# Optimization experiments

Measured on AMD Instinct MI355X. Metric: run time of the kernel, lower is better.

## Reference

```python
import jax, jax.numpy as jnp
import numpy as np

N = 4096
E = 262144
IN_DIM = 256
EDGE_DIM = 16
NUM_ATOM_FEATURES = 16
LATENT_DIM = 128
NUM_BOND_TYPES = 5


def setup_inputs() -> dict:
    key = jax.random.key(0)
    ks = jax.random.split(key, 12)
    inp = {
        's': jax.random.normal(ks[0], (N, IN_DIM), dtype=jnp.float32),
        'e': jax.random.normal(ks[1], (E, EDGE_DIM), dtype=jnp.float32),
        'batch': jnp.zeros((N,), dtype=jnp.int64),
        'edge_index_global': jax.random.randint(ks[2], (2, E), 0, N, dtype=jnp.int64),
        # learned parameters (torch nn.Linear layout: W is [out, in])
        'W_shared': jax.random.normal(ks[3], (IN_DIM, IN_DIM), dtype=jnp.float32) * 0.02,
        'b_shared': jnp.zeros((IN_DIM,), dtype=jnp.float32),
        'W_bond': jax.random.normal(ks[4], (IN_DIM, EDGE_DIM), dtype=jnp.float32) * 0.02,
        'b_bond': jnp.zeros((IN_DIM,), dtype=jnp.float32),
        'W_bonds': jax.random.normal(ks[5], (NUM_BOND_TYPES, IN_DIM), dtype=jnp.float32) * 0.02,
        'b_bonds': jnp.zeros((NUM_BOND_TYPES,), dtype=jnp.float32),
        'W_atoms': jax.random.normal(ks[6], (NUM_ATOM_FEATURES + LATENT_DIM, IN_DIM), dtype=jnp.float32) * 0.02,
        'b_atoms': jnp.zeros((NUM_ATOM_FEATURES + LATENT_DIM,), dtype=jnp.float32),
    }
    return inp


def reference(s, e, batch, edge_index_global,
              W_shared, b_shared, W_bond, b_bond,
              W_bonds, b_bonds, W_atoms, b_atoms):
    # shared_mapping: Linear + SiLU
    s = jax.nn.silu(s @ W_shared.T + b_shared)  # [n, in_dim]
    j = edge_index_global[0]
    i = edge_index_global[1]
    n = s.shape[0]

    # atoms_lin then split into atom-type logits and latent prediction
    atoms_out = s @ W_atoms.T + b_atoms  # [n, num_atom_features + latent_dim]
    atoms_pred = atoms_out[:, :NUM_ATOM_FEATURES]
    latent_pred = atoms_out[:, NUM_ATOM_FEATURES:]

    # dense scatter -> symmetrize -> gather (faithful to the original O(n^2) path)
    e_dense = jnp.zeros((n, n, e.shape[-1]), dtype=e.dtype).at[j, i].set(e)
    e_dense = 0.5 * (e_dense + e_dense.transpose(1, 0, 2))
    e_sym = e_dense[j, i]  # [E, edge_dim]

    # fused gather + bond linear + SiLU + bonds linear
    f = jax.nn.silu(s[i] + s[j] + e_sym @ W_bond.T + b_bond)  # [E, in_dim]
    bonds_pred = f @ W_bonds.T + b_bonds  # [E, num_bond_types]

    return (latent_pred, atoms_pred, bonds_pred)
```

## Files before the change

### kernel.cpp

```cpp
#include <hip/hip_runtime.h>
#include <hip/hip_bf16.h>

#define N_NODES   4096
#define E_EDGES   262144
#define IN_DIM    256
#define EDGE_DIM  16
#define NAF       16
#define LATENT    128
#define NBT       5

#define LATENT_OFF 0
#define ATOMS_OFF  (N_NODES * LATENT)
#define BONDS_OFF  (ATOMS_OFF + N_NODES * NAF)

#define TBITS 20
#define TSIZE (1u << TBITS)
#define TMASK (TSIZE - 1u)

typedef float    f32x4  __attribute__((ext_vector_type(4)));
typedef float    f32x4v __attribute__((ext_vector_type(4)));
typedef short    bf16x8 __attribute__((ext_vector_type(8)));
typedef unsigned u32x2  __attribute__((ext_vector_type(2)));
typedef unsigned u32x4  __attribute__((ext_vector_type(4)));

__device__ __forceinline__ float silu_f(float x) {
    return x * __builtin_amdgcn_rcpf(1.0f + __expf(-x));
}

__device__ __forceinline__ unsigned pack_bf16x2(float lo, float hi) {
#if __has_builtin(__builtin_amdgcn_cvt_pk_bf16_f32)
    typedef __bf16 bf16x2_t __attribute__((ext_vector_type(2)));
    union { bf16x2_t v; unsigned u; } c;
    c.v = __builtin_amdgcn_cvt_pk_bf16_f32(lo, hi);
    return c.u;
#else
    union { float f; unsigned u; } a, b;
    a.f = lo; b.f = hi;
    const unsigned ra = (a.u + 0x7FFFu + ((a.u >> 16) & 1u)) >> 16;
    const unsigned rb = (b.u + 0x7FFFu + ((b.u >> 16) & 1u)) >> 16;
    return ra | (rb << 16);
#endif
}

__device__ __forceinline__ float bf_lo(unsigned u) {
    union { unsigned x; float f; } c; c.x = u << 16; return c.f;
}
__device__ __forceinline__ float bf_hi(unsigned u) {
    union { unsigned x; float f; } c; c.x = u & 0xFFFF0000u; return c.f;
}

__device__ __forceinline__ void split_bf16(const float4 x0, const float4 x1,
                                           bf16x8* hi, bf16x8* lo) {
    union { bf16x8 v; unsigned u[4]; } H, L;
    H.u[0] = pack_bf16x2(x0.x, x0.y);
    H.u[1] = pack_bf16x2(x0.z, x0.w);
    H.u[2] = pack_bf16x2(x1.x, x1.y);
    H.u[3] = pack_bf16x2(x1.z, x1.w);
    L.u[0] = pack_bf16x2(x0.x - bf_lo(H.u[0]), x0.y - bf_hi(H.u[0]));
    L.u[1] = pack_bf16x2(x0.z - bf_lo(H.u[1]), x0.w - bf_hi(H.u[1]));
    L.u[2] = pack_bf16x2(x1.x - bf_lo(H.u[2]), x1.y - bf_hi(H.u[2]));
    L.u[3] = pack_bf16x2(x1.z - bf_lo(H.u[3]), x1.w - bf_hi(H.u[3]));
    *hi = H.v; *lo = L.v;
}

__device__ __forceinline__ void gld_lds16(const void* g, void* l) {
    __builtin_amdgcn_global_load_lds(
        (const __attribute__((address_space(1))) unsigned*)g,
        (__attribute__((address_space(3))) unsigned*)l, 16, 0, 0);
}

__device__ __forceinline__ unsigned hashh(unsigned key) {
    return (key * 2654435761u) >> (32 - TBITS);
}

__device__ __forceinline__ int resolve2(const unsigned long long* __restrict__ tab,
                                        unsigned key, unsigned long long s0,
                                        unsigned long long s1, unsigned h) {
    if ((unsigned)(s0 >> 18) == key + 1u) return (int)(s0 & 0x3FFFFu);
    if (s0 == 0ULL) return -1;
    if ((unsigned)(s1 >> 18) == key + 1u) return (int)(s1 & 0x3FFFFu);
    if (s1 == 0ULL) return -1;
    h = (h + 2u) & TMASK;
    while (true) {
        const unsigned long long cur = tab[h];
        if (cur == 0ULL) return -1;
        if ((unsigned)(cur >> 18) == key + 1u) return (int)(cur & 0x3FFFFu);
        h = (h + 1u) & TMASK;
    }
}

__global__ __launch_bounds__(256) void k_front(const float* __restrict__ s,
                                               const float* __restrict__ Wsh,
                                               const float* __restrict__ bsh,
                                               const int* __restrict__ eidx,
                                               const float* __restrict__ Wb,
                                               const float* __restrict__ bb,
                                               const float* __restrict__ Wbs,
                                               unsigned short* __restrict__ sact16,
                                               unsigned long long* __restrict__ tab,
                                               u32x4* __restrict__ A1pre,
                                               u32x4* __restrict__ A2pre) {
    const int blk = blockIdx.x;
    const int c   = threadIdx.x;

    if (blk >= 1024) {
        if (blk < 2048) {
            const int k = (blk - 1024) * 256 + c;
            const unsigned j = (unsigned)eidx[k];
            const unsigned i = (unsigned)eidx[E_EDGES + k];
            const unsigned key = (j << 12) | i;
            const unsigned long long mine =
                ((unsigned long long)(key + 1u) << 18) | (unsigned)k;
            unsigned h = hashh(key);
            while (true) {
                unsigned long long cur = tab[h];
                if (cur == 0ULL) {
                    const unsigned long long old = atomicCAS(&tab[h], 0ULL, mine);
                    if (old == 0ULL) return;
                    cur = old;
                }
                if ((unsigned)(cur >> 18) == key + 1u) {
                    atomicMax(&tab[h], mine);
                    return;
                }
                h = (h + 1u) & TMASK;
            }
        } else {
#pragma unroll
            for (int ee = 0; ee < 4; ++ee) {
                const int idx  = c + 256 * ee;
                const int g    = idx >> 6;
                const int lane = idx & 63;
                const int mm   = lane & 15;
                const int qq   = lane >> 4;

                const float4 w = *(const float4*)(Wb + (16 * g + mm) * EDGE_DIM + 4 * qq);
                u32x4 r1;
                r1.x = pack_bf16x2(w.x, w.y);
                r1.y = pack_bf16x2(w.z, w.w);
                r1.z = pack_bf16x2(bb[16 * g + mm], 0.0f);
                r1.w = 0u;
                A1pre[idx] = r1;

                u32x4 r2;
                if (mm < NBT) {
                    const float4 ws = *(const float4*)(Wbs + mm * IN_DIM + 16 * g + 4 * qq);
                    r2.x = pack_bf16x2(ws.x, ws.y);
                    r2.y = pack_bf16x2(ws.z, ws.w);
                } else {
                    r2.x = 0u; r2.y = 0u;
                }
                r2.z = 0u; r2.w = 0u;
                A2pre[idx] = r2;
            }
        }
        return;
    }

    const int lane = c & 63;
    const int wv   = c >> 6;
    const int wave = blk * 4 + wv;
    const int m    = lane & 15;
    const int q    = lane >> 4;
    const int row0 = (wave >> 4) * 16;
    const int col0 = (wave & 15) * 16;

    f32x4v acc;
    {
        const float bias = bsh[col0 + m];
        acc[0] = bias; acc[1] = bias; acc[2] = bias; acc[3] = bias;
    }

    const float* ap = s   + (size_t)(row0 + m) * IN_DIM + 8 * q;
    const float* bp = Wsh + (size_t)(col0 + m) * IN_DIM + 8 * q;

#pragma unroll
    for (int c8 = 0; c8 < 8; ++c8) {
        const float4 a0 = *(const float4*)(ap + 32 * c8);
        const float4 a1 = *(const float4*)(ap + 32 * c8 + 4);
        const float4 b0 = *(const float4*)(bp + 32 * c8);
        const float4 b1 = *(const float4*)(bp + 32 * c8 + 4);
        bf16x8 Ah, Al, Bh, Bl;
        split_bf16(a0, a1, &Ah, &Al);
        split_bf16(b0, b1, &Bh, &Bl);
        acc = __builtin_amdgcn_mfma_f32_16x16x32_bf16(Ah, Bh, acc, 0, 0, 0);
        acc = __builtin_amdgcn_mfma_f32_16x16x32_bf16(Al, Bh, acc, 0, 0, 0);
        acc = __builtin_amdgcn_mfma_f32_16x16x32_bf16(Ah, Bl, acc, 0, 0, 0);
    }

#pragma unroll
    for (int r = 0; r < 4; ++r) {
        const int row = row0 + 4 * q + r;
        const float v = silu_f(acc[r]);
        sact16[(size_t)row * IN_DIM + col0 + m] =
            (unsigned short)(pack_bf16x2(v, 0.0f) & 0xFFFFu);
    }
}

#define SB0()    __builtin_amdgcn_sched_barrier(0)
#define LGKM0()  do { __asm__ __volatile__("s_waitcnt lgkmcnt(0)" ::: "memory"); SB0(); } while (0)
#define VMW(n)   do { __asm__ __volatile__("s_waitcnt vmcnt(" #n ")" ::: "memory"); SB0(); } while (0)

__global__ __launch_bounds__(256, 5) void k_edges_mfma(const int* __restrict__ eidx,
                                                       const float* __restrict__ e,
                                                       const unsigned long long* __restrict__ tab,
                                                       const unsigned short* __restrict__ sact16,
                                                       const u32x4* __restrict__ A1pre,
                                                       const u32x4* __restrict__ A2pre,
                                                       const float* __restrict__ bbs,
                                                       const float* __restrict__ Wa,
                                                       const float* __restrict__ ba,
                                                       float* __restrict__ out) {
    __shared__ unsigned lds_all[4][2048];
    const int blk  = blockIdx.x;
    const int lane = threadIdx.x & 63;
    const int wv   = threadIdx.x >> 6;
    const int m    = lane & 15;
    const int q    = lane >> 4;

    if (blk >= 4096) {
        const int wave = (blk - 4096) * 4 + wv;
        const int rt = wave / 9;
        const int ct = wave - rt * 9;
        const int row0  = rt * 16;
        const int n_abs = ct * 16 + m;

        f32x4v acc;
        {
            const float bias = ba[n_abs];
            acc[0] = bias; acc[1] = bias; acc[2] = bias; acc[3] = bias;
        }

        const unsigned short* apu = sact16 + (size_t)(row0 + m) * IN_DIM + 8 * q;
        const float*          bp  = Wa + (size_t)n_abs * IN_DIM + 8 * q;

#pragma unroll
        for (int c8 = 0; c8 < 8; ++c8) {
            const bf16x8 A = *(const bf16x8*)(apu + 32 * c8);
            const float4 b0 = *(const float4*)(bp + 32 * c8);
            const float4 b1 = *(const float4*)(bp + 32 * c8 + 4);
            bf16x8 Bh, Bl;
            split_bf16(b0, b1, &Bh, &Bl);
            acc = __builtin_amdgcn_mfma_f32_16x16x32_bf16(A, Bh, acc, 0, 0, 0);
            acc = __builtin_amdgcn_mfma_f32_16x16x32_bf16(A, Bl, acc, 0, 0, 0);
        }
#pragma unroll
        for (int r = 0; r < 4; ++r) {
            const int row = row0 + 4 * q + r;
            if (n_abs < NAF)
                out[ATOMS_OFF + (size_t)row * NAF + n_abs] = acc[r];
            else
                out[LATENT_OFF + (size_t)row * LATENT + (n_abs - NAF)] = acc[r];
        }
        return;
    }

    const int k0 = __builtin_amdgcn_readfirstlane((blk * 4 + wv) * 16);
    unsigned* myl = lds_all[wv];
    const short one_q0 = (q == 0) ? (short)0x3F80 : (short)0;

    f32x4v acc_init;
#pragma unroll
    for (int r = 0; r < 4; ++r) {
        const int bond = 4 * q + r;
        acc_init[r] = (bond < NBT) ? bbs[bond] : 0.0f;
    }
    const u32x4* a1p = A1pre + lane;
    const u32x4* a2p = A2pre + lane;
    const int qh = q >> 1;
    const int qw = 2 * (q & 1);
    const int mw = m * 4;

    const unsigned j_m = (unsigned)eidx[k0 + m];
    const unsigned i_m = (unsigned)eidx[E_EDGES + k0 + m];

    const char* si_base = (const char*)(sact16 + (size_t)i_m * IN_DIM);
    const char* sj_base = (const char*)(sact16 + (size_t)j_m * IN_DIM);

    const unsigned keyF = (j_m << 12) | i_m, keyR = (i_m << 12) | j_m;
    const unsigned hF = hashh(keyF), hR = hashh(keyR);
    const unsigned long long sF0 = tab[hF];
    const unsigned long long sF1 = tab[(hF + 1u) & TMASK];
    const unsigned long long sR0 = tab[hR];
    const unsigned long long sR1 = tab[(hR + 1u) & TMASK];

    auto stage_q = [&](int p, int qb) {
        gld_lds16(si_base + p * 128 + (q)     * 16, (char*)myl + qb);
        gld_lds16(si_base + p * 128 + (4 + q) * 16, (char*)myl + qb + 1024);
        gld_lds16(sj_base + p * 128 + (q)     * 16, (char*)myl + qb + 2048);
        gld_lds16(sj_base + p * 128 + (4 + q) * 16, (char*)myl + qb + 3072);
        SB0();
    };

    stage_q(0, 0);
    stage_q(1, 4096);

    const int wf = resolve2(tab, keyF, sF0, sF1, hF);
    const int wr = resolve2(tab, keyR, sR0, sR1, hR);

    const float rsc = (wr >= 0) ? 0.5f : 0.0f;
    const int   wrc = (wr >= 0) ? wr : 0;
    const f32x4 ef = *(const f32x4*)(e + (size_t)wf  * EDGE_DIM + 4 * q);
    const f32x4 er = *(const f32x4*)(e + (size_t)wrc * EDGE_DIM + 4 * q);

    union { bf16x8 v; short s[8]; unsigned u[4]; } B1;
    {
        const f32x4 es = ef * 0.5f + er * rsc;
        B1.u[0] = pack_bf16x2(es[0], es[1]);
        B1.u[1] = pack_bf16x2(es[2], es[3]);
        B1.s[4] = one_q0; B1.s[5] = 0;
        B1.u[3] = 0u;
    }

    f32x4v acc0 = acc_init;
    f32x4v acc1 = {0.0f, 0.0f, 0.0f, 0.0f};

    auto qcompute = [&](int qb4, int gbase) {
#pragma unroll
        for (int gp = 0; gp < 4; ++gp) {
            const int g   = gbase + gp;
            const int cl  = 2 * gp + qh;
            const int off = (cl >> 2) * 256 + (cl & 3) * 64 + mw + qw;

            const u32x2 wi = *(const u32x2*)(myl + qb4 + off);
            const u32x2 wj = *(const u32x2*)(myl + qb4 + 512 + off);

            f32x4v C1;
            C1[0] = bf_lo(wi.x) + bf_lo(wj.x);
            C1[1] = bf_hi(wi.x) + bf_hi(wj.x);
            C1[2] = bf_lo(wi.y) + bf_lo(wj.y);
            C1[3] = bf_hi(wi.y) + bf_hi(wj.y);

            const u32x4 r1 = a1p[g * 64];
            const u32x4 r2 = a2p[g * 64];
            union { bf16x8 v; unsigned u[4]; } A1, A2;
            A1.u[0] = r1.x; A1.u[1] = r1.y; A1.u[2] = r1.z; A1.u[3] = 0u;
            A2.u[0] = r2.x; A2.u[1] = r2.y; A2.u[2] = 0u;   A2.u[3] = 0u;

            const f32x4v P = __builtin_amdgcn_mfma_f32_16x16x32_bf16(A1.v, B1.v, C1, 0, 0, 0);

            union { bf16x8 v; unsigned u[4]; } B2;
            B2.u[0] = pack_bf16x2(silu_f(P[0]), silu_f(P[1]));
            B2.u[1] = pack_bf16x2(silu_f(P[2]), silu_f(P[3]));
            B2.u[2] = 0u; B2.u[3] = 0u;

            if (gp & 1) acc1 = __builtin_amdgcn_mfma_f32_16x16x32_bf16(A2.v, B2.v, acc1, 0, 0, 0);
            else        acc0 = __builtin_amdgcn_mfma_f32_16x16x32_bf16(A2.v, B2.v, acc0, 0, 0, 0);
        }
    };

    VMW(0);
    qcompute(0, 0);
    LGKM0();
    stage_q(2, 0);

    qcompute(1024, 4);
    LGKM0();
    stage_q(3, 4096);

    VMW(4);
    qcompute(0, 8);

    VMW(0);
    qcompute(1024, 12);

    const f32x4v accT = acc0 + acc1;
    float* op = out + BONDS_OFF + (size_t)(k0 + m) * NBT;
    if (q == 0) {
        __builtin_nontemporal_store(accT[0], op + 0);
        __builtin_nontemporal_store(accT[1], op + 1);
        __builtin_nontemporal_store(accT[2], op + 2);
        __builtin_nontemporal_store(accT[3], op + 3);
    } else if (q == 1) {
        __builtin_nontemporal_store(accT[0], op + 4);
    }
}

extern "C" void kernel_launch(void* const* d_in, const int* in_sizes, int n_in,
                              void* d_out, int out_size, void* d_ws, size_t ws_size,
                              hipStream_t stream) {
    const float* s   = (const float*)d_in[0];
    const float* e   = (const float*)d_in[1];
    const int*   eix = (const int*)d_in[3];
    const float* Wsh = (const float*)d_in[4];
    const float* bsh = (const float*)d_in[5];
    const float* Wb  = (const float*)d_in[6];
    const float* bbo = (const float*)d_in[7];
    const float* Wbs = (const float*)d_in[8];
    const float* bbs = (const float*)d_in[9];
    const float* Wa  = (const float*)d_in[10];
    const float* ba  = (const float*)d_in[11];
    float* out = (float*)d_out;

    char* ws = (char*)d_ws;
    unsigned short*     sact16 = (unsigned short*)ws;
    u32x4*              A1pre  = (u32x4*)(ws + (2u << 20));
    u32x4*              A2pre  = (u32x4*)(ws + (2u << 20) + 16384);
    unsigned long long* tab    = (unsigned long long*)(ws + (3u << 20));

    (void)hipMemsetAsync(tab, 0x00, TSIZE * sizeof(unsigned long long), stream);

    k_front<<<2049, 256, 0, stream>>>(s, Wsh, bsh, eix, Wb, bbo, Wbs,
                                      sact16, tab, A1pre, A2pre);
    k_edges_mfma<<<4672, 256, 0, stream>>>(eix, e, tab, sact16,
                                           A1pre, A2pre, bbs, Wa, ba, out);
}
```

Baseline: 181.9 us.

## Process two edge tiles per wave with cross-tile prefetch; use direct CAS in hash insert

Each wave in the edge kernel now handles two 16-edge tiles instead of one. It issues the hash probes for both tiles up front and starts staging the second tile's gathered rows and resolving its edge features while the first tile's MFMAs are still running. This is meant to hide gather and hash-lookup latency and to cut per-block setup cost, at the price of more registers and half as many blocks. The hash insert in the front kernel also drops the pre-read and goes straight to atomicCAS.

```diff
diff --git a/kernel.cpp b/kernel.cpp
--- a/kernel.cpp
+++ b/kernel.cpp
@@ -113,13 +113,9 @@
                 ((unsigned long long)(key + 1u) << 18) | (unsigned)k;
             unsigned h = hashh(key);
             while (true) {
-                unsigned long long cur = tab[h];
-                if (cur == 0ULL) {
-                    const unsigned long long old = atomicCAS(&tab[h], 0ULL, mine);
-                    if (old == 0ULL) return;
-                    cur = old;
-                }
-                if ((unsigned)(cur >> 18) == key + 1u) {
+                const unsigned long long old = atomicCAS(&tab[h], 0ULL, mine);
+                if (old == 0ULL) return;
+                if ((unsigned)(old >> 18) == key + 1u) {
                     atomicMax(&tab[h], mine);
                     return;
                 }
@@ -218,8 +214,8 @@
     const int m    = lane & 15;
     const int q    = lane >> 4;
 
-    if (blk >= 4096) {
-        const int wave = (blk - 4096) * 4 + wv;
+    if (blk >= 2048) {
+        const int wave = (blk - 2048) * 4 + wv;
         const int rt = wave / 9;
         const int ct = wave - rt * 9;
         const int row0  = rt * 16;
@@ -255,8 +251,10 @@
         return;
     }
 
-    const int k0 = __builtin_amdgcn_readfirstlane((blk * 4 + wv) * 16);
-    unsigned* myl = lds_all[wv];
+    const int wave = blk * 4 + wv;
+    const int ka   = __builtin_amdgcn_readfirstlane(wave * 32);
+    const int kb   = ka + 16;
+    unsigned* myl  = lds_all[wv];
     const short one_q0 = (q == 0) ? (short)0x3F80 : (short)0;
 
     f32x4v acc_init;
@@ -271,51 +269,61 @@
     const int qw = 2 * (q & 1);
     const int mw = m * 4;
 
-    const unsigned j_m = (unsigned)eidx[k0 + m];
-    const unsigned i_m = (unsigned)eidx[E_EDGES + k0 + m];
-
-    const char* si_base = (const char*)(sact16 + (size_t)i_m * IN_DIM);
-    const char* sj_base = (const char*)(sact16 + (size_t)j_m * IN_DIM);
-
-    const unsigned keyF = (j_m << 12) | i_m, keyR = (i_m << 12) | j_m;
-    const unsigned hF = hashh(keyF), hR = hashh(keyR);
-    const unsigned long long sF0 = tab[hF];
-    const unsigned long long sF1 = tab[(hF + 1u) & TMASK];
-    const unsigned long long sR0 = tab[hR];
-    const unsigned long long sR1 = tab[(hR + 1u) & TMASK];
-
-    auto stage_q = [&](int p, int qb) {
-        gld_lds16(si_base + p * 128 + (q)     * 16, (char*)myl + qb);
-        gld_lds16(si_base + p * 128 + (4 + q) * 16, (char*)myl + qb + 1024);
-        gld_lds16(sj_base + p * 128 + (q)     * 16, (char*)myl + qb + 2048);
-        gld_lds16(sj_base + p * 128 + (4 + q) * 16, (char*)myl + qb + 3072);
+    const unsigned jA = (unsigned)eidx[ka + m];
+    const unsigned iA = (unsigned)eidx[E_EDGES + ka + m];
+    const unsigned jB = (unsigned)eidx[kb + m];
+    const unsigned iB = (unsigned)eidx[E_EDGES + kb + m];
+
+    const char* siA = (const char*)(sact16 + (size_t)iA * IN_DIM);
+    const char* sjA = (const char*)(sact16 + (size_t)jA * IN_DIM);
+    const char* siB = (const char*)(sact16 + (size_t)iB * IN_DIM);
+    const char* sjB = (const char*)(sact16 + (size_t)jB * IN_DIM);
+
+    const unsigned keyFA = (jA << 12) | iA, keyRA = (iA << 12) | jA;
+    const unsigned keyFB = (jB << 12) | iB, keyRB = (iB << 12) | jB;
+    const unsigned hFA = hashh(keyFA), hRA = hashh(keyRA);
+    const unsigned hFB = hashh(keyFB), hRB = hashh(keyRB);
+
+    const unsigned long long sFA0 = tab[hFA];
+    const unsigned long long sFA1 = tab[(hFA + 1u) & TMASK];
+    const unsigned long long sRA0 = tab[hRA];
+    const unsigned long long sRA1 = tab[(hRA + 1u) & TMASK];
+    const unsigned long long sFB0 = tab[hFB];
+    const unsigned long long sFB1 = tab[(hFB + 1u) & TMASK];
+    const unsigned long long sRB0 = tab[hRB];
+    const unsigned long long sRB1 = tab[(hRB + 1u) & TMASK];
+
+    auto stage_q = [&](const char* si_b, const char* sj_b, int p, int qb) {
+        gld_lds16(si_b + p * 128 + (q)     * 16, (char*)myl + qb);
+        gld_lds16(si_b + p * 128 + (4 + q) * 16, (char*)myl + qb + 1024);
+        gld_lds16(sj_b + p * 128 + (q)     * 16, (char*)myl + qb + 2048);
+        gld_lds16(sj_b + p * 128 + (4 + q) * 16, (char*)myl + qb + 3072);
         SB0();
     };
 
-    stage_q(0, 0);
-    stage_q(1, 4096);
-
-    const int wf = resolve2(tab, keyF, sF0, sF1, hF);
-    const int wr = resolve2(tab, keyR, sR0, sR1, hR);
-
-    const float rsc = (wr >= 0) ? 0.5f : 0.0f;
-    const int   wrc = (wr >= 0) ? wr : 0;
-    const f32x4 ef = *(const f32x4*)(e + (size_t)wf  * EDGE_DIM + 4 * q);
-    const f32x4 er = *(const f32x4*)(e + (size_t)wrc * EDGE_DIM + 4 * q);
-
-    union { bf16x8 v; short s[8]; unsigned u[4]; } B1;
+    stage_q(siA, sjA, 0, 0);
+    stage_q(siA, sjA, 1, 4096);
+
+    const int wfA = resolve2(tab, keyFA, sFA0, sFA1, hFA);
+    const int wrA = resolve2(tab, keyRA, sRA0, sRA1, hRA);
+    const float rscA = (wrA >= 0) ? 0.5f : 0.0f;
+    const int   wrcA = (wrA >= 0) ? wrA : 0;
+    const f32x4 efA = *(const f32x4*)(e + (size_t)wfA  * EDGE_DIM + 4 * q);
+    const f32x4 erA = *(const f32x4*)(e + (size_t)wrcA * EDGE_DIM + 4 * q);
+
+    union { bf16x8 v; short s[8]; unsigned u[4]; } B1A;
     {
-        const f32x4 es = ef * 0.5f + er * rsc;
-        B1.u[0] = pack_bf16x2(es[0], es[1]);
-        B1.u[1] = pack_bf16x2(es[2], es[3]);
-        B1.s[4] = one_q0; B1.s[5] = 0;
-        B1.u[3] = 0u;
+        const f32x4 es = efA * 0.5f + erA * rscA;
+        B1A.u[0] = pack_bf16x2(es[0], es[1]);
+        B1A.u[1] = pack_bf16x2(es[2], es[3]);
+        B1A.s[4] = one_q0; B1A.s[5] = 0;
+        B1A.u[3] = 0u;
     }
 
     f32x4v acc0 = acc_init;
     f32x4v acc1 = {0.0f, 0.0f, 0.0f, 0.0f};
 
-    auto qcompute = [&](int qb4, int gbase) {
+    auto qcompute = [&](int qb4, int gbase, const bf16x8 B1v) {
 #pragma unroll
         for (int gp = 0; gp < 4; ++gp) {
             const int g   = gbase + gp;
@@ -337,7 +345,7 @@
             A1.u[0] = r1.x; A1.u[1] = r1.y; A1.u[2] = r1.z; A1.u[3] = 0u;
             A2.u[0] = r2.x; A2.u[1] = r2.y; A2.u[2] = 0u;   A2.u[3] = 0u;
 
-            const f32x4v P = __builtin_amdgcn_mfma_f32_16x16x32_bf16(A1.v, B1.v, C1, 0, 0, 0);
+            const f32x4v P = __builtin_amdgcn_mfma_f32_16x16x32_bf16(A1.v, B1v, C1, 0, 0, 0);
 
             union { bf16x8 v; unsigned u[4]; } B2;
             B2.u[0] = pack_bf16x2(silu_f(P[0]), silu_f(P[1]));
@@ -349,31 +357,74 @@
         }
     };
 
+    auto store_bonds = [&](int k0, const f32x4v accT) {
+        float* op = out + BONDS_OFF + (size_t)(k0 + m) * NBT;
+        if (q == 0) {
+            __builtin_nontemporal_store(accT[0], op + 0);
+            __builtin_nontemporal_store(accT[1], op + 1);
+            __builtin_nontemporal_store(accT[2], op + 2);
+            __builtin_nontemporal_store(accT[3], op + 3);
+        } else if (q == 1) {
+            __builtin_nontemporal_store(accT[0], op + 4);
+        }
+    };
+
+    VMW(2);
+    qcompute(0, 0, B1A.v);
+    LGKM0();
+    stage_q(siA, sjA, 2, 0);
+
+    qcompute(1024, 4, B1A.v);
+    LGKM0();
+    stage_q(siA, sjA, 3, 4096);
+
+    VMW(4);
+    qcompute(0, 8, B1A.v);
+    LGKM0();
+    stage_q(siB, sjB, 0, 0);
+
+    const int wfB = resolve2(tab, keyFB, sFB0, sFB1, hFB);
+    const int wrB = resolve2(tab, keyRB, sRB0, sRB1, hRB);
+    const float rscB = (wrB >= 0) ? 0.5f : 0.0f;
+    const int   wrcB = (wrB >= 0) ? wrB : 0;
+    const f32x4 efB = *(const f32x4*)(e + (size_t)wfB  * EDGE_DIM + 4 * q);
+    const f32x4 erB = *(const f32x4*)(e + (size_t)wrcB * EDGE_DIM + 4 * q);
+
+    VMW(6);
+    qcompute(1024, 12, B1A.v);
+    LGKM0();
+    stage_q(siB, sjB, 1, 4096);
+
+    store_bonds(ka, acc0 + acc1);
+
+    union { bf16x8 v; short s[8]; unsigned u[4]; } B1B;
+    {
+        const f32x4 es = efB * 0.5f + erB * rscB;
+        B1B.u[0] = pack_bf16x2(es[0], es[1]);
+        B1B.u[1] = pack_bf16x2(es[2], es[3]);
+        B1B.s[4] = one_q0; B1B.s[5] = 0;
+        B1B.u[3] = 0u;
+    }
+    acc0 = acc_init;
+    acc1 = (f32x4v){0.0f, 0.0f, 0.0f, 0.0f};
+
+    VMW(4);
+    qcompute(0, 0, B1B.v);
+    LGKM0();
+    stage_q(siB, sjB, 2, 0);
+
+    VMW(4);
+    qcompute(1024, 4, B1B.v);
+    LGKM0();
+    stage_q(siB, sjB, 3, 4096);
+
+    VMW(4);
+    qcompute(0, 8, B1B.v);
+
     VMW(0);
-    qcompute(0, 0);
-    LGKM0();
-    stage_q(2, 0);
-
-    qcompute(1024, 4);
-    LGKM0();
-    stage_q(3, 4096);
-
-    VMW(4);
-    qcompute(0, 8);
-
-    VMW(0);
-    qcompute(1024, 12);
-
-    const f32x4v accT = acc0 + acc1;
-    float* op = out + BONDS_OFF + (size_t)(k0 + m) * NBT;
-    if (q == 0) {
-        __builtin_nontemporal_store(accT[0], op + 0);
-        __builtin_nontemporal_store(accT[1], op + 1);
-        __builtin_nontemporal_store(accT[2], op + 2);
-        __builtin_nontemporal_store(accT[3], op + 3);
-    } else if (q == 1) {
-        __builtin_nontemporal_store(accT[0], op + 4);
-    }
+    qcompute(1024, 12, B1B.v);
+
+    store_bonds(kb, acc0 + acc1);
 }
 
 extern "C" void kernel_launch(void* const* d_in, const int* in_sizes, int n_in,
@@ -402,6 +453,6 @@
 
     k_front<<<2049, 256, 0, stream>>>(s, Wsh, bsh, eix, Wb, bbo, Wbs,
                                       sact16, tab, A1pre, A2pre);
-    k_edges_mfma<<<4672, 256, 0, stream>>>(eix, e, tab, sact16,
+    k_edges_mfma<<<2624, 256, 0, stream>>>(eix, e, tab, sact16,
                                            A1pre, A2pre, bbs, Wa, ba, out);
 }
```

Result: slower. 218.4 us (+20.0%).

## Halve LDS staging chunks and deepen edge pipeline for higher occupancy

Applied to the files above, without the earlier changes.

The edge kernel now stages the gathered s[i]/s[j] rows into LDS in 64-byte chunks instead of 128-byte chunks. This halves per-block LDS so the launch bound can rise from 5 to 8 blocks per CU, and the pipeline becomes eight smaller stages with double buffering. The hash insert also drops the pre-read and goes straight to atomicCAS. The trade-off is more wait and sync points per edge and a tighter register budget, which could cause spills.

```diff
diff --git a/kernel.cpp b/kernel.cpp
--- a/kernel.cpp
+++ b/kernel.cpp
@@ -113,13 +113,9 @@
                 ((unsigned long long)(key + 1u) << 18) | (unsigned)k;
             unsigned h = hashh(key);
             while (true) {
-                unsigned long long cur = tab[h];
-                if (cur == 0ULL) {
-                    const unsigned long long old = atomicCAS(&tab[h], 0ULL, mine);
-                    if (old == 0ULL) return;
-                    cur = old;
-                }
-                if ((unsigned)(cur >> 18) == key + 1u) {
+                const unsigned long long old = atomicCAS(&tab[h], 0ULL, mine);
+                if (old == 0ULL) return;
+                if ((unsigned)(old >> 18) == key + 1u) {
                     atomicMax(&tab[h], mine);
                     return;
                 }
@@ -201,7 +197,7 @@
 #define LGKM0()  do { __asm__ __volatile__("s_waitcnt lgkmcnt(0)" ::: "memory"); SB0(); } while (0)
 #define VMW(n)   do { __asm__ __volatile__("s_waitcnt vmcnt(" #n ")" ::: "memory"); SB0(); } while (0)
 
-__global__ __launch_bounds__(256, 5) void k_edges_mfma(const int* __restrict__ eidx,
+__global__ __launch_bounds__(256, 8) void k_edges_mfma(const int* __restrict__ eidx,
                                                        const float* __restrict__ e,
                                                        const unsigned long long* __restrict__ tab,
                                                        const unsigned short* __restrict__ sact16,
@@ -211,7 +207,7 @@
                                                        const float* __restrict__ Wa,
                                                        const float* __restrict__ ba,
                                                        float* __restrict__ out) {
-    __shared__ unsigned lds_all[4][2048];
+    __shared__ unsigned lds_all[4][1024];
     const int blk  = blockIdx.x;
     const int lane = threadIdx.x & 63;
     const int wv   = threadIdx.x >> 6;
@@ -284,16 +280,14 @@
     const unsigned long long sR0 = tab[hR];
     const unsigned long long sR1 = tab[(hR + 1u) & TMASK];
 
-    auto stage_q = [&](int p, int qb) {
-        gld_lds16(si_base + p * 128 + (q)     * 16, (char*)myl + qb);
-        gld_lds16(si_base + p * 128 + (4 + q) * 16, (char*)myl + qb + 1024);
-        gld_lds16(sj_base + p * 128 + (q)     * 16, (char*)myl + qb + 2048);
-        gld_lds16(sj_base + p * 128 + (4 + q) * 16, (char*)myl + qb + 3072);
+    auto stage_e = [&](int p, int qb) {
+        gld_lds16(si_base + p * 64 + q * 16, (char*)myl + qb);
+        gld_lds16(sj_base + p * 64 + q * 16, (char*)myl + qb + 1024);
         SB0();
     };
 
-    stage_q(0, 0);
-    stage_q(1, 4096);
+    stage_e(0, 0);
+    stage_e(1, 2048);
 
     const int wf = resolve2(tab, keyF, sF0, sF1, hF);
     const int wr = resolve2(tab, keyR, sR0, sR1, hR);
@@ -315,15 +309,14 @@
     f32x4v acc0 = acc_init;
     f32x4v acc1 = {0.0f, 0.0f, 0.0f, 0.0f};
 
-    auto qcompute = [&](int qb4, int gbase) {
-#pragma unroll
-        for (int gp = 0; gp < 4; ++gp) {
+    auto qcompute2 = [&](int qb4, int gbase) {
+#pragma unroll
+        for (int gp = 0; gp < 2; ++gp) {
             const int g   = gbase + gp;
-            const int cl  = 2 * gp + qh;
-            const int off = (cl >> 2) * 256 + (cl & 3) * 64 + mw + qw;
+            const int off = (2 * gp + qh) * 64 + mw + qw;
 
             const u32x2 wi = *(const u32x2*)(myl + qb4 + off);
-            const u32x2 wj = *(const u32x2*)(myl + qb4 + 512 + off);
+            const u32x2 wj = *(const u32x2*)(myl + qb4 + 256 + off);
 
             f32x4v C1;
             C1[0] = bf_lo(wi.x) + bf_lo(wj.x);
@@ -350,19 +343,33 @@
     };
 
     VMW(0);
-    qcompute(0, 0);
-    LGKM0();
-    stage_q(2, 0);
-
-    qcompute(1024, 4);
-    LGKM0();
-    stage_q(3, 4096);
-
-    VMW(4);
-    qcompute(0, 8);
+    qcompute2(0, 0);
+    LGKM0(); stage_e(2, 0);
+
+    qcompute2(512, 2);
+    LGKM0(); stage_e(3, 2048);
+
+    VMW(2);
+    qcompute2(0, 4);
+    LGKM0(); stage_e(4, 0);
+
+    VMW(2);
+    qcompute2(512, 6);
+    LGKM0(); stage_e(5, 2048);
+
+    VMW(2);
+    qcompute2(0, 8);
+    LGKM0(); stage_e(6, 0);
+
+    VMW(2);
+    qcompute2(512, 10);
+    LGKM0(); stage_e(7, 2048);
+
+    VMW(2);
+    qcompute2(0, 12);
 
     VMW(0);
-    qcompute(1024, 12);
+    qcompute2(512, 14);
 
     const f32x4v accT = acc0 + acc1;
     float* op = out + BONDS_OFF + (size_t)(k0 + m) * NBT;
```

Result: faster. 175.1 us (-3.7%).
